# Kernel optimization log

Measured on AMD Instinct MI355X. Metric: run time of the kernel, lower is better.

## Reference

```python
import jax, jax.numpy as jnp
import numpy as np
import math

B, S, HID, NH = 2, 1024, 4096, 32
HD = HID // NH  # 128


def setup_inputs() -> dict:
    key = jax.random.key(0)
    ks = jax.random.split(key, 6)
    scale = 0.02
    x = jax.random.normal(ks[0], (B, S, HID), dtype=jnp.float32)
    Wq = jax.random.normal(ks[1], (HID, HID), dtype=jnp.float32) * scale
    Wk = jax.random.normal(ks[2], (HID, HID), dtype=jnp.float32) * scale
    Wv = jax.random.normal(ks[3], (HID, HID), dtype=jnp.float32) * scale
    Wo = jax.random.normal(ks[4], (HID, HID), dtype=jnp.float32) * scale
    bq = jnp.zeros((HID,), jnp.float32)
    bk = jnp.zeros((HID,), jnp.float32)
    bv = jnp.zeros((HID,), jnp.float32)
    bo = jnp.zeros((HID,), jnp.float32)
    position_ids = jnp.tile(jnp.arange(S, dtype=jnp.int32)[None, :], (B, 1))
    # additive causal mask: 0 on/below diagonal, large negative above
    causal = jnp.tril(jnp.ones((S, S), dtype=bool))
    attention_mask = jnp.where(causal, 0.0, -1e9).astype(jnp.float32)[None, None]
    return {"x": x, "Wq": Wq, "bq": bq, "Wk": Wk, "bk": bk, "Wv": Wv,
            "bv": bv, "Wo": Wo, "bo": bo, "position_ids": position_ids,
            "attention_mask": attention_mask}


def _rotate_interleaved(t):
    # stack([-t[..., 1::2], t[..., ::2]], -1).reshape_as(t)
    return jnp.stack([-t[..., 1::2], t[..., ::2]], axis=-1).reshape(t.shape)


def reference(x, Wq, bq, Wk, bk, Wv, bv, Wo, bo, position_ids, attention_mask):
    b, s, _ = x.shape
    q = x @ Wq.T + bq
    k = x @ Wk.T + bk
    v = x @ Wv.T + bv
    # [B, NH, S, HD]
    q = q.reshape(b, s, NH, HD).transpose(0, 2, 1, 3)
    k = k.reshape(b, s, NH, HD).transpose(0, 2, 1, 3)
    v = v.reshape(b, s, NH, HD).transpose(0, 2, 1, 3)
    # RoPE (interleaved pairs), cos/sin recomputed each call as in source
    inv_freq = 1.0 / (10000.0 ** (jnp.arange(0, HD, 2, dtype=jnp.float32) / HD))
    ang = position_ids.astype(jnp.float32)[..., None] * inv_freq  # [B,S,HD/2]
    cos = jnp.repeat(jnp.cos(ang), 2, axis=-1)[:, None]  # [B,1,S,HD]
    sin = jnp.repeat(jnp.sin(ang), 2, axis=-1)[:, None]
    q = q * cos + _rotate_interleaved(q) * sin
    k = k * cos + _rotate_interleaved(k) * sin
    # naive full attention
    scores = jnp.einsum('bhqd,bhkd->bhqk', q, k) / math.sqrt(HD)
    scores = scores + attention_mask
    probs = jax.nn.softmax(scores, axis=-1)
    out = jnp.einsum('bhqk,bhkd->bhqd', probs, v)
    out = out.transpose(0, 2, 1, 3).reshape(b, s, HID)
    return out @ Wo.T + bo
```

## Files before the change

### kernel.cpp

```cpp
#include <hip/hip_runtime.h>
#include <hip/hip_bf16.h>
#include <cmath>

constexpr int cB  = 2;
constexpr int cS  = 1024;
constexpr int cNH = 32;
constexpr int cHD = 128;
constexpr int cHID = 4096;
constexpr int cM  = cB * cS;

typedef unsigned short u16;
typedef __bf16 bf16x8 __attribute__((ext_vector_type(8)));
typedef float  f32x4  __attribute__((ext_vector_type(4)));

__device__ __forceinline__ u16 f2b(float f) { return __builtin_bit_cast(u16, (__bf16)f); }

__global__ void cvt_bf16(const float* __restrict__ in, u16* __restrict__ out, int n8) {
  int i = blockIdx.x * blockDim.x + threadIdx.x;
  if (i >= n8) return;
  const float4* in4 = (const float4*)in;
  float4 a = in4[2 * i], b = in4[2 * i + 1];
  union { u16 u[8]; uint4 v; } r;
  r.u[0] = f2b(a.x); r.u[1] = f2b(a.y); r.u[2] = f2b(a.z); r.u[3] = f2b(a.w);
  r.u[4] = f2b(b.x); r.u[5] = f2b(b.y); r.u[6] = f2b(b.z); r.u[7] = f2b(b.w);
  ((uint4*)out)[i] = r.v;
}

__global__ void rope_table_k(const int* __restrict__ pos,
                             float* __restrict__ cosT, float* __restrict__ sinT) {
  int idx = blockIdx.x * blockDim.x + threadIdx.x;
  int i = idx & 63, bs = idx >> 6;
  float p = (float)pos[bs];
  float freq = exp2f(-(float)i * (13.287712379549449f / 64.0f));
  float a = p * freq;
  float s, c;
  sincosf(a, &s, &c);
  cosT[idx] = c; sinT[idx] = s;
}

__global__ void rope_apply(u16* __restrict__ Q, u16* __restrict__ Kb,
                           const float* __restrict__ cosT, const float* __restrict__ sinT) {
  int idx = blockIdx.x * blockDim.x + threadIdx.x;
  const int nPer = cB * cS * cNH * (cHD / 8);
  u16* P = (idx < nPer) ? Q : Kb;
  int t = (idx < nPer) ? idx : idx - nPer;
  int d8 = t & 15;
  int h  = (t >> 4) & 31;
  int bs = t >> 9;
  size_t base = ((size_t)bs * cNH + h) * cHD + d8 * 8;
  uint4 v = *reinterpret_cast<uint4*>(P + base);
  u16* u = reinterpret_cast<u16*>(&v);
  int pb = bs * 64 + d8 * 4;
  float4 cs = *reinterpret_cast<const float4*>(cosT + pb);
  float4 sn = *reinterpret_cast<const float4*>(sinT + pb);
  float co[4] = {cs.x, cs.y, cs.z, cs.w};
  float si[4] = {sn.x, sn.y, sn.z, sn.w};
#pragma unroll
  for (int p = 0; p < 4; ++p) {
    float e = (float)__builtin_bit_cast(__bf16, u[2 * p]);
    float o = (float)__builtin_bit_cast(__bf16, u[2 * p + 1]);
    float e2 = e * co[p] - o * si[p];
    float o2 = o * co[p] + e * si[p];
    u[2 * p]     = f2b(e2);
    u[2 * p + 1] = f2b(o2);
  }
  *reinterpret_cast<uint4*>(P + base) = v;
}

__global__ void transpose_v(const u16* __restrict__ V, u16* __restrict__ Vt) {
  __shared__ u16 tile[32][33];
  int bh = blockIdx.z;
  int b = bh >> 5, h = bh & 31;
  int s0 = blockIdx.x * 32, d0 = blockIdx.y * 32;
  int tx = threadIdx.x & 31, ty0 = threadIdx.x >> 5;
#pragma unroll
  for (int i = 0; i < 4; ++i) {
    int r = ty0 + i * 8;
    tile[r][tx] = V[((size_t)(b * cS + s0 + r) * cNH + h) * cHD + d0 + tx];
  }
  __syncthreads();
#pragma unroll
  for (int i = 0; i < 4; ++i) {
    int r = ty0 + i * 8;
    Vt[((size_t)bh * cHD + d0 + r) * cS + s0 + tx] = tile[tx][r];
  }
}

template <int MODE>
__global__ __launch_bounds__(512, 2)
void gemm8(const u16* __restrict__ A,
           const u16* __restrict__ W0, const u16* __restrict__ W1,
           const u16* __restrict__ W2,
           const float* __restrict__ b0, const float* __restrict__ b1,
           const float* __restrict__ b2,
           void* o0, void* o1, void* o2) {
  __shared__ __align__(16) u16 sA[3][128 * 64];
  __shared__ __align__(16) u16 sB[3][256 * 64];
  const int tid = threadIdx.x;
  const int wid = tid >> 6, lane = tid & 63;
  const int c = lane & 15, g = lane >> 4;
  const int wm = wid >> 2, wn = wid & 3;
  const int m0 = blockIdx.x * 128;
  const int gn0 = blockIdx.y * 256;
  const int sel = gn0 >> 12;
  const int n0 = gn0 & 4095;
  const u16* Bw = (sel == 0) ? W0 : (sel == 1 ? W1 : W2);

  f32x4 acc[4][4] = {};
  const int nkt = cHID / 64;

#define STAGE_A(kt, dst)                                                       \
  {                                                                            \
    _Pragma("unroll") for (int l = 0; l < 2; ++l) {                            \
      int chunk = (l * 8 + wid) * 64 + lane;                                   \
      int row = chunk >> 3, kc = (chunk & 7) ^ (row & 7);                      \
      __builtin_amdgcn_global_load_lds(                                        \
          (const void*)(A + (size_t)(m0 + row) * cHID + (kt) * 64 + kc * 8),   \
          (void*)(&sA[dst][(l * 8 + wid) * 512]), 16, 0, 0);                   \
    }                                                                          \
  }
#define STAGE_B(kt, dst)                                                       \
  {                                                                            \
    _Pragma("unroll") for (int l = 0; l < 4; ++l) {                            \
      int chunk = (l * 8 + wid) * 64 + lane;                                   \
      int row = chunk >> 3, kc = (chunk & 7) ^ (row & 7);                      \
      __builtin_amdgcn_global_load_lds(                                        \
          (const void*)(Bw + (size_t)(n0 + row) * cHID + (kt) * 64 + kc * 8),  \
          (void*)(&sB[dst][(l * 8 + wid) * 512]), 16, 0, 0);                   \
    }                                                                          \
  }

  STAGE_A(0, 0); STAGE_B(0, 0);
  STAGE_A(1, 1); STAGE_B(1, 1);
  asm volatile("s_waitcnt vmcnt(6)" ::: "memory");
  __builtin_amdgcn_sched_barrier(0);
  __builtin_amdgcn_s_barrier();
  asm volatile("" ::: "memory");
  __builtin_amdgcn_sched_barrier(0);

  for (int kt = 0; kt < nkt; ++kt) {
    const int bufR = kt % 3;
    const int bufW = (kt + 2) % 3;
    const bool doStage = (kt + 2) < nkt;

    bf16x8 af[4], bw[4];
#pragma unroll
    for (int mf = 0; mf < 4; ++mf) {
      int ra = wm * 64 + mf * 16 + c;
      af[mf] = *reinterpret_cast<const bf16x8*>(
          &sA[bufR][ra * 64 + ((g ^ (ra & 7)) * 8)]);
    }
#pragma unroll
    for (int nf = 0; nf < 4; ++nf) {
      int rb = wn * 64 + nf * 16 + c;
      bw[nf] = *reinterpret_cast<const bf16x8*>(
          &sB[bufR][rb * 64 + ((g ^ (rb & 7)) * 8)]);
    }
    if (doStage) STAGE_A(kt + 2, bufW);
    __builtin_amdgcn_s_setprio(1);
#pragma unroll
    for (int mf = 0; mf < 4; ++mf)
#pragma unroll
      for (int nf = 0; nf < 4; ++nf)
        acc[mf][nf] = __builtin_amdgcn_mfma_f32_16x16x32_bf16(af[mf], bw[nf], acc[mf][nf], 0, 0, 0);
    __builtin_amdgcn_s_setprio(0);

#pragma unroll
    for (int mf = 0; mf < 4; ++mf) {
      int ra = wm * 64 + mf * 16 + c;
      af[mf] = *reinterpret_cast<const bf16x8*>(
          &sA[bufR][ra * 64 + (((4 + g) ^ (ra & 7)) * 8)]);
    }
#pragma unroll
    for (int nf = 0; nf < 4; ++nf) {
      int rb = wn * 64 + nf * 16 + c;
      bw[nf] = *reinterpret_cast<const bf16x8*>(
          &sB[bufR][rb * 64 + (((4 + g) ^ (rb & 7)) * 8)]);
    }
    if (doStage) STAGE_B(kt + 2, bufW);
    __builtin_amdgcn_s_setprio(1);
#pragma unroll
    for (int mf = 0; mf < 4; ++mf)
#pragma unroll
      for (int nf = 0; nf < 4; ++nf)
        acc[mf][nf] = __builtin_amdgcn_mfma_f32_16x16x32_bf16(af[mf], bw[nf], acc[mf][nf], 0, 0, 0);
    __builtin_amdgcn_s_setprio(0);

    if (doStage) {
      asm volatile("s_waitcnt vmcnt(6)" ::: "memory");
    } else {
      asm volatile("s_waitcnt vmcnt(0)" ::: "memory");
    }
    __builtin_amdgcn_sched_barrier(0);
    __builtin_amdgcn_s_barrier();
    asm volatile("" ::: "memory");
    __builtin_amdgcn_sched_barrier(0);
  }
#undef STAGE_A
#undef STAGE_B

  const float* bp = (sel == 0) ? b0 : (sel == 1 ? b1 : b2);
  void* op = (sel == 0) ? o0 : (sel == 1 ? o1 : o2);
#pragma unroll
  for (int nf = 0; nf < 4; ++nf) {
    int col = n0 + wn * 64 + nf * 16 + c;
    float bv = bp[col];
#pragma unroll
    for (int mf = 0; mf < 4; ++mf) {
      int row = m0 + wm * 64 + mf * 16 + g * 4;
#pragma unroll
      for (int r = 0; r < 4; ++r) {
        float v = acc[mf][nf][r] + bv;
        if (MODE == 0)
          ((u16*)op)[(size_t)(row + r) * cHID + col] = f2b(v);
        else
          ((float*)op)[(size_t)(row + r) * cHID + col] = v;
      }
    }
  }
}

__global__ __launch_bounds__(256, 2)
void attn_kernel(const u16* __restrict__ Q, const u16* __restrict__ Kb,
                 const u16* __restrict__ Vt, u16* __restrict__ O) {
  __shared__ __align__(16) char sK[2][16384];
  __shared__ __align__(16) char sV[2][16384];
  __shared__ __align__(16) char sP[8192];
  const int tid = threadIdx.x, w = tid >> 6, lane = tid & 63;
  const int c = lane & 15, g = lane >> 4;
  const int bh = blockIdx.y;
  const int b = bh >> 5, h = bh & 31;
  const int NT = cS / 64;
  const int qtA = blockIdx.x, qtB = NT - 1 - blockIdx.x;
  const float kSc = 0.12751744f;

  bf16x8 qf[2][4];
#pragma unroll
  for (int s = 0; s < 2; ++s) {
    int q0s = (s ? qtA : qtB) * 64;
    size_t qrow = ((size_t)(b * cS + q0s + w * 16 + c) * cNH + h) * cHD;
#pragma unroll
    for (int df = 0; df < 4; ++df)
      qf[s][df] = *reinterpret_cast<const bf16x8*>(Q + qrow + df * 32 + g * 8);
  }

  f32x4 o[2][8] = {};
  float mx[2][4], ls[2][4];
#pragma unroll
  for (int s = 0; s < 2; ++s)
#pragma unroll
    for (int r = 0; r < 4; ++r) { mx[s][r] = -1e30f; ls[s][r] = 0.f; }

  uint4 kv[4], vv[4];
#define LOADT(t)                                                               \
  {                                                                            \
    _Pragma("unroll") for (int i = 0; i < 4; ++i) {                            \
      int cidx = i * 256 + tid;                                                \
      { int row = cidx >> 4, ch = cidx & 15;                                   \
        kv[i] = *reinterpret_cast<const uint4*>(                               \
            Kb + ((size_t)(b * cS + (t) * 64 + row) * cNH + h) * cHD + ch * 8); } \
      { int row = cidx >> 3, ch = cidx & 7;                                    \
        vv[i] = *reinterpret_cast<const uint4*>(                               \
            Vt + ((size_t)bh * cHD + row) * cS + (t) * 64 + ch * 8); }         \
    }                                                                          \
  }
#define WRITET(buf)                                                            \
  {                                                                            \
    _Pragma("unroll") for (int i = 0; i < 4; ++i) {                            \
      int cidx = i * 256 + tid;                                                \
      { int row = cidx >> 4, ch = cidx & 15;                                   \
        *reinterpret_cast<uint4*>(sK[buf] + row * 256 + ((ch ^ (row & 7)) * 16)) = kv[i]; } \
      { int row = cidx >> 3, ch = cidx & 7;                                    \
        *reinterpret_cast<uint4*>(sV[buf] + row * 128 + ((ch ^ (row & 7)) * 16)) = vv[i]; } \
    }                                                                          \
  }

  LOADT(0);
  WRITET(0);
  int cur = 0;

  for (int t = 0; t <= qtB; ++t) {
    __syncthreads();
    if (t < qtB) LOADT(t + 1);

#pragma unroll
    for (int s = 0; s < 2; ++s) {
      const int qt_s = s ? qtA : qtB;
      if (t > qt_s) continue;
      const int q0_s = qt_s * 64;

      f32x4 sc[4] = {};
#pragma unroll
      for (int df = 0; df < 4; ++df) {
        bf16x8 kb[4];
#pragma unroll
        for (int cf = 0; cf < 4; ++cf) {
          int kr = cf * 16 + c;
          kb[cf] = *reinterpret_cast<const bf16x8*>(sK[cur] + kr * 256 + (((df * 4 + g) ^ (kr & 7)) * 16));
        }
#pragma unroll
        for (int cf = 0; cf < 4; ++cf)
          sc[cf] = __builtin_amdgcn_mfma_f32_16x16x32_bf16(qf[s][df], kb[cf], sc[cf], 0, 0, 0);
      }

      if (t == qt_s) {
#pragma unroll
        for (int cf = 0; cf < 4; ++cf) {
          int kg = t * 64 + cf * 16 + c;
#pragma unroll
          for (int r = 0; r < 4; ++r) {
            int qg = q0_s + w * 16 + g * 4 + r;
            if (kg > qg) sc[cf][r] = -1e30f;
          }
        }
      }

      float alpha[4];
#pragma unroll
      for (int r = 0; r < 4; ++r) {
        float v = fmaxf(fmaxf(sc[0][r], sc[1][r]), fmaxf(sc[2][r], sc[3][r]));
        v = fmaxf(v, __shfl_xor(v, 1));
        v = fmaxf(v, __shfl_xor(v, 2));
        v = fmaxf(v, __shfl_xor(v, 4));
        v = fmaxf(v, __shfl_xor(v, 8));
        float mn = fmaxf(mx[s][r], v);
        alpha[r] = exp2f((mx[s][r] - mn) * kSc);
        mx[s][r] = mn;
      }
      float rs[4] = {0.f, 0.f, 0.f, 0.f};
#pragma unroll
      for (int cf = 0; cf < 4; ++cf)
#pragma unroll
        for (int r = 0; r < 4; ++r) {
          float p = exp2f((sc[cf][r] - mx[s][r]) * kSc);
          sc[cf][r] = p;
          rs[r] += p;
        }
#pragma unroll
      for (int r = 0; r < 4; ++r) {
        float v = rs[r];
        v += __shfl_xor(v, 1); v += __shfl_xor(v, 2);
        v += __shfl_xor(v, 4); v += __shfl_xor(v, 8);
        ls[s][r] = ls[s][r] * alpha[r] + v;
      }
#pragma unroll
      for (int nf = 0; nf < 8; ++nf)
#pragma unroll
        for (int r = 0; r < 4; ++r)
          o[s][nf][r] *= alpha[r];

      char* myP = sP + w * 2048;
#pragma unroll
      for (int cf = 0; cf < 4; ++cf) {
        int kcol = cf * 16 + c;
        int chunk = kcol >> 3, within = kcol & 7;
#pragma unroll
        for (int r = 0; r < 4; ++r) {
          int qr = g * 4 + r;
          *reinterpret_cast<u16*>(myP + qr * 128 + ((chunk ^ (qr & 7)) * 16) + within * 2) =
              f2b(sc[cf][r]);
        }
      }
      bf16x8 pa[2];
#pragma unroll
      for (int kf = 0; kf < 2; ++kf)
        pa[kf] = *reinterpret_cast<const bf16x8*>(myP + c * 128 + (((kf * 4 + g) ^ (c & 7)) * 16));

#pragma unroll
      for (int kf = 0; kf < 2; ++kf) {
#pragma unroll
        for (int nf = 0; nf < 8; ++nf) {
          int dr = nf * 16 + c;
          bf16x8 vb = *reinterpret_cast<const bf16x8*>(sV[cur] + dr * 128 + (((kf * 4 + g) ^ (dr & 7)) * 16));
          o[s][nf] = __builtin_amdgcn_mfma_f32_16x16x32_bf16(pa[kf], vb, o[s][nf], 0, 0, 0);
        }
      }
    }

    if (t < qtB) { WRITET(cur ^ 1); cur ^= 1; }
  }

  __syncthreads();
#pragma unroll
  for (int s = 0; s < 2; ++s) {
#pragma unroll
    for (int nf = 0; nf < 8; ++nf) {
#pragma unroll
      for (int r = 0; r < 4; ++r) {
        float v = o[s][nf][r] / ls[s][r];
        int qr = w * 16 + g * 4 + r;
        *reinterpret_cast<u16*>(sK[s] + qr * 256 + (nf * 16 + c) * 2) = f2b(v);
      }
    }
  }
  __syncthreads();
#pragma unroll
  for (int s = 0; s < 2; ++s) {
    int q0_s = (s ? qtA : qtB) * 64;
#pragma unroll
    for (int i = 0; i < 4; ++i) {
      int cidx = i * 256 + tid;
      int row = cidx >> 4, ch = cidx & 15;
      uint4 v = *reinterpret_cast<const uint4*>(sK[s] + row * 256 + ch * 16);
      *reinterpret_cast<uint4*>(O + ((size_t)(b * cS + q0_s + row) * cNH + h) * cHD + ch * 8) = v;
    }
  }
#undef LOADT
#undef WRITET
}

extern "C" void kernel_launch(void* const* d_in, const int* in_sizes, int n_in,
                              void* d_out, int out_size, void* d_ws, size_t ws_size,
                              hipStream_t stream) {
  const float* x  = (const float*)d_in[0];
  const float* Wq = (const float*)d_in[1];
  const float* bq = (const float*)d_in[2];
  const float* Wk = (const float*)d_in[3];
  const float* bk = (const float*)d_in[4];
  const float* Wv = (const float*)d_in[5];
  const float* bv = (const float*)d_in[6];
  const float* Wo = (const float*)d_in[7];
  const float* bo = (const float*)d_in[8];
  const int*  pos = (const int*)d_in[9];
  float* out = (float*)d_out;

  char* ws = (char*)d_ws;
  const size_t MB = 1u << 20;
  const int W8 = (cHID * cHID) / 8;
  const int X8 = (cM * cHID) / 8;
  const int R8 = cB * cS * cNH * (cHD / 8);

  if (ws_size >= 168 * MB) {
    u16* xb  = (u16*)(ws);
    u16* Qb  = (u16*)(ws + 16 * MB);
    u16* Kb  = (u16*)(ws + 32 * MB);
    u16* Vb  = (u16*)(ws + 48 * MB);
    float* cosT = (float*)(ws + 64 * MB);
    float* sinT = cosT + cB * cS * 64;
    u16* WbQ = (u16*)(ws + 72 * MB);
    u16* WbK = (u16*)(ws + 104 * MB);
    u16* WbV = (u16*)(ws + 136 * MB);
    u16* Vt  = WbQ;
    u16* Ab  = WbK;
    u16* WbO = WbV;

    cvt_bf16<<<X8 / 256, 256, 0, stream>>>(x, xb, X8);
    cvt_bf16<<<W8 / 256, 256, 0, stream>>>(Wq, WbQ, W8);
    cvt_bf16<<<W8 / 256, 256, 0, stream>>>(Wk, WbK, W8);
    cvt_bf16<<<W8 / 256, 256, 0, stream>>>(Wv, WbV, W8);
    rope_table_k<<<(cB * cS * 64) / 256, 256, 0, stream>>>(pos, cosT, sinT);

    gemm8<0><<<dim3(16, 48), 512, 0, stream>>>(
        xb, WbQ, WbK, WbV, bq, bk, bv, Qb, Kb, Vb);

    rope_apply<<<(2 * R8) / 256, 256, 0, stream>>>(Qb, Kb, cosT, sinT);
    transpose_v<<<dim3(cS / 32, cHD / 32, cB * cNH), 256, 0, stream>>>(Vb, Vt);
    attn_kernel<<<dim3(cS / 128, cB * cNH), 256, 0, stream>>>(Qb, Kb, Vt, Ab);

    cvt_bf16<<<W8 / 256, 256, 0, stream>>>(Wo, WbO, W8);
    gemm8<1><<<dim3(16, 16), 512, 0, stream>>>(
        Ab, WbO, WbO, WbO, bo, bo, bo, out, out, out);
  } else {
    u16* xb = (u16*)(ws);
    u16* Wb = (u16*)(ws + 16 * MB);
    u16* Qb = (u16*)(ws + 48 * MB);
    u16* Kb = (u16*)(ws + 64 * MB);
    u16* Vb = (u16*)(ws + 80 * MB);
    u16* Vt = xb;
    u16* Ab = Vb;
    float* cosT = (float*)(ws + 96 * MB);
    float* sinT = cosT + cB * cS * 64;

    cvt_bf16<<<X8 / 256, 256, 0, stream>>>(x, xb, X8);
    cvt_bf16<<<W8 / 256, 256, 0, stream>>>(Wq, Wb, W8);
    gemm8<0><<<dim3(16, 16), 512, 0, stream>>>(
        xb, Wb, Wb, Wb, bq, bq, bq, Qb, Qb, Qb);
    cvt_bf16<<<W8 / 256, 256, 0, stream>>>(Wk, Wb, W8);
    gemm8<0><<<dim3(16, 16), 512, 0, stream>>>(
        xb, Wb, Wb, Wb, bk, bk, bk, Kb, Kb, Kb);
    cvt_bf16<<<W8 / 256, 256, 0, stream>>>(Wv, Wb, W8);
    gemm8<0><<<dim3(16, 16), 512, 0, stream>>>(
        xb, Wb, Wb, Wb, bv, bv, bv, Vb, Vb, Vb);

    rope_table_k<<<(cB * cS * 64) / 256, 256, 0, stream>>>(pos, cosT, sinT);
    rope_apply<<<(2 * R8) / 256, 256, 0, stream>>>(Qb, Kb, cosT, sinT);
    transpose_v<<<dim3(cS / 32, cHD / 32, cB * cNH), 256, 0, stream>>>(Vb, Vt);
    attn_kernel<<<dim3(cS / 128, cB * cNH), 256, 0, stream>>>(Qb, Kb, Vt, Ab);

    cvt_bf16<<<W8 / 256, 256, 0, stream>>>(Wo, Wb, W8);
    gemm8<1><<<dim3(16, 16), 512, 0, stream>>>(
        Ab, Wb, Wb, Wb, bo, bo, bo, out, out, out);
  }
}
```

Baseline: 472.8 us.

## Add 256x256-tile GEMM with XCD-aware block mapping and split-K output projection

Replaces the 128x256-tile GEMM with a new 256x256-tile kernel that loads global data straight into LDS with swizzling, double-buffers LDS with explicit waitcnt/barrier scheduling, and maps blocks so that each XCD owns a contiguous group of N tiles. The QKV projection runs as one 384-block launch. The output projection splits K in two, writes fp32 partials to the workspace, and adds a combine_bias kernel that sums them with the bias. The aim is more operand reuse per tile, better L2 locality per XCD, and better occupancy on the smaller output GEMM. The cost is an extra fp32 partial write and read plus one more kernel launch.

```diff
diff --git a/kernel.cpp b/kernel.cpp
--- a/kernel.cpp
+++ b/kernel.cpp
@@ -84,6 +84,176 @@
     int r = ty0 + i * 8;
     Vt[((size_t)bh * cHD + d0 + r) * cS + s0 + tx] = tile[tx][r];
   }
+}
+
+template <int MODE, int NTX>
+__global__ __launch_bounds__(512, 2)
+void gemm256(const u16* __restrict__ A_,
+             const u16* __restrict__ W0, const u16* __restrict__ W1,
+             const u16* __restrict__ W2,
+             const float* __restrict__ b0_, const float* __restrict__ b1_,
+             const float* __restrict__ b2_,
+             void* o0, void* o1, void* o2, int ktiles) {
+  __shared__ __align__(16) u16 sm[2][4][8192];
+  const int tid = threadIdx.x, wid = tid >> 6, lane = tid & 63;
+  const int c = lane & 15, g = lane >> 4;
+  const int wm = wid >> 2, wn = wid & 3;
+  const int gsw = (g ^ ((c >> 1) & 3)) * 8;
+  const int bid = blockIdx.x;
+  const int xcd = bid & 7, j = bid >> 3;
+  const int mt = j / NTX, ntl = xcd * NTX + j % NTX;
+  const int mrow0 = mt * 256;
+  const int gn0 = ntl * 256;
+  const int sel = gn0 >> 12;
+  const int n0 = gn0 & 4095;
+  const u16* Bw = (sel == 0) ? W0 : (sel == 1 ? W1 : W2);
+  const int kbase = blockIdx.y * ktiles * 64;
+
+  f32x4 acc[8][4] = {};
+
+#define STG(P, R0, T, KKH, DD, U)                                              \
+  {                                                                            \
+    _Pragma("unroll") for (int l = 0; l < 2; ++l) {                            \
+      int ci = (l * 8 + wid) * 64 + lane;                                      \
+      int rw = ci >> 2;                                                        \
+      int kc2 = (ci & 3) ^ ((rw >> 1) & 3);                                    \
+      __builtin_amdgcn_global_load_lds(                                        \
+          (const void*)((P) + (size_t)((R0) + rw) * cHID + kbase + (T) * 64 +  \
+                        (KKH) * 32 + kc2 * 8),                                 \
+          (void*)(&sm[DD][U][(l * 8 + wid) * 512]), 16, 0, 0);                 \
+    }                                                                          \
+  }
+
+#define RD_A(dst, MH, UU, DD)                                                  \
+  _Pragma("unroll") for (int i = 0; i < 4; ++i) {                              \
+    int ra = wm * 128 + (MH) * 64 + i * 16 + c;                                \
+    dst[i] = *reinterpret_cast<const bf16x8*>(&sm[DD][UU][ra * 32 + gsw]);     \
+  }
+#define RD_B(dst, UU, DD)                                                      \
+  _Pragma("unroll") for (int i = 0; i < 4; ++i) {                              \
+    int rb = wn * 64 + i * 16 + c;                                             \
+    dst[i] = *reinterpret_cast<const bf16x8*>(&sm[DD][UU][rb * 32 + gsw]);     \
+  }
+#define MFMA16(aR, bR, MOFF)                                                   \
+  __builtin_amdgcn_s_setprio(1);                                               \
+  _Pragma("unroll") for (int i = 0; i < 4; ++i)                                \
+    _Pragma("unroll") for (int nf = 0; nf < 4; ++nf)                           \
+      acc[(MOFF) + i][nf] =                                                    \
+          __builtin_amdgcn_mfma_f32_16x16x32_bf16(aR[i], bR[nf],               \
+                                                  acc[(MOFF) + i][nf], 0, 0, 0); \
+  __builtin_amdgcn_s_setprio(0);
+#define LEADBAR                                                                \
+  __builtin_amdgcn_s_barrier();                                                \
+  asm volatile("s_waitcnt lgkmcnt(0)" ::: "memory");                           \
+  __builtin_amdgcn_sched_barrier(0)
+#define TRAILBAR                                                               \
+  __builtin_amdgcn_s_barrier();                                                \
+  __builtin_amdgcn_sched_barrier(0)
+
+#define GTILE(DD, KT, SON, LAST)                                               \
+  {                                                                            \
+    bf16x8 aR[4], bk0[4], bk1[4];                                              \
+                                                   \
+    RD_A(aR, 0, 0, DD); RD_B(bk0, 1, DD);                                      \
+    if (SON) STG(A_, mrow0, (KT) + 1, 0, (DD) ^ 1, 0);                         \
+    LEADBAR;                                                                   \
+    MFMA16(aR, bk0, 0);                                                        \
+    TRAILBAR;                                                                  \
+                                                   \
+    RD_A(aR, 1, 0, DD);                                                        \
+    if (SON) STG(Bw, n0, (KT) + 1, 0, (DD) ^ 1, 1);                            \
+    LEADBAR;                                                                   \
+    MFMA16(aR, bk0, 4);                                                        \
+    if (LAST) { asm volatile("s_waitcnt vmcnt(0)" ::: "memory"); }             \
+    else      { asm volatile("s_waitcnt vmcnt(4)" ::: "memory"); }             \
+    __builtin_amdgcn_sched_barrier(0);                                         \
+    TRAILBAR;                                                                  \
+                                                   \
+    RD_A(aR, 0, 2, DD); RD_B(bk1, 3, DD);                                      \
+    if (SON) STG(A_, mrow0, (KT) + 1, 1, (DD) ^ 1, 2);                         \
+    LEADBAR;                                                                   \
+    MFMA16(aR, bk1, 0);                                                        \
+    TRAILBAR;                                                                  \
+                                                   \
+    RD_A(aR, 1, 2, DD);                                                        \
+    if (SON) STG(Bw, n0, (KT) + 1, 1, (DD) ^ 1, 3);                            \
+    LEADBAR;                                                                   \
+    MFMA16(aR, bk1, 4);                                                        \
+    if (SON) {                                                                 \
+      asm volatile("s_waitcnt vmcnt(4)" ::: "memory");                         \
+      __builtin_amdgcn_sched_barrier(0);                                       \
+    }                                                                          \
+    TRAILBAR;                                                                  \
+  }
+
+  STG(A_, mrow0, 0, 0, 0, 0);
+  STG(Bw, n0, 0, 0, 0, 1);
+  STG(A_, mrow0, 0, 1, 0, 2);
+  STG(Bw, n0, 0, 1, 0, 3);
+  asm volatile("s_waitcnt vmcnt(4)" ::: "memory");
+  __builtin_amdgcn_sched_barrier(0);
+  __builtin_amdgcn_s_barrier();
+  __builtin_amdgcn_sched_barrier(0);
+
+  for (int kt = 0; kt < ktiles - 1; ++kt) {
+    const int D = kt & 1;
+    GTILE(D, kt, 1, 0);
+  }
+  {
+    const int D = (ktiles - 1) & 1;
+    GTILE(D, ktiles - 1, 0, 1);
+  }
+#undef GTILE
+#undef STG
+#undef RD_A
+#undef RD_B
+#undef MFMA16
+#undef LEADBAR
+#undef TRAILBAR
+
+  const float* bp = (sel == 0) ? b0_ : (sel == 1 ? b1_ : b2_);
+  void* op = (sel == 0) ? o0 : (sel == 1 ? o1 : o2);
+  if (MODE == 0) {
+#pragma unroll
+    for (int nf = 0; nf < 4; ++nf) {
+      int col = n0 + wn * 64 + nf * 16 + c;
+      float bv = bp[col];
+#pragma unroll
+      for (int mf = 0; mf < 8; ++mf) {
+        int row = mrow0 + wm * 128 + mf * 16 + g * 4;
+#pragma unroll
+        for (int r = 0; r < 4; ++r)
+          ((u16*)op)[(size_t)(row + r) * cHID + col] = f2b(acc[mf][nf][r] + bv);
+      }
+    }
+  } else {
+    float* fp = (float*)op + (size_t)blockIdx.y * cM * cHID;
+#pragma unroll
+    for (int nf = 0; nf < 4; ++nf) {
+      int col = n0 + wn * 64 + nf * 16 + c;
+#pragma unroll
+      for (int mf = 0; mf < 8; ++mf) {
+        int row = mrow0 + wm * 128 + mf * 16 + g * 4;
+#pragma unroll
+        for (int r = 0; r < 4; ++r)
+          fp[(size_t)(row + r) * cHID + col] = acc[mf][nf][r];
+      }
+    }
+  }
+}
+
+__global__ void combine_bias(const float* __restrict__ P,
+                             const float* __restrict__ bias,
+                             float* __restrict__ out) {
+  int i = blockIdx.x * blockDim.x + threadIdx.x;
+  float4 a = ((const float4*)P)[i];
+  float4 b = ((const float4*)P)[i + (cM * cHID / 4)];
+  int col4 = (i & (cHID / 4 - 1)) * 4;
+  float4 bb = *reinterpret_cast<const float4*>(bias + col4);
+  float4 r;
+  r.x = a.x + b.x + bb.x; r.y = a.y + b.y + bb.y;
+  r.z = a.z + b.z + bb.z; r.w = a.w + b.w + bb.w;
+  ((float4*)out)[i] = r;
 }
 
 template <int MODE>
@@ -443,6 +613,7 @@
     u16* Vt  = WbQ;
     u16* Ab  = WbK;
     u16* WbO = WbV;
+    float* P01 = (float*)(ws);
 
     cvt_bf16<<<X8 / 256, 256, 0, stream>>>(x, xb, X8);
     cvt_bf16<<<W8 / 256, 256, 0, stream>>>(Wq, WbQ, W8);
@@ -450,16 +621,17 @@
     cvt_bf16<<<W8 / 256, 256, 0, stream>>>(Wv, WbV, W8);
     rope_table_k<<<(cB * cS * 64) / 256, 256, 0, stream>>>(pos, cosT, sinT);
 
-    gemm8<0><<<dim3(16, 48), 512, 0, stream>>>(
-        xb, WbQ, WbK, WbV, bq, bk, bv, Qb, Kb, Vb);
+    gemm256<0, 6><<<dim3(384), 512, 0, stream>>>(
+        xb, WbQ, WbK, WbV, bq, bk, bv, Qb, Kb, Vb, 64);
 
     rope_apply<<<(2 * R8) / 256, 256, 0, stream>>>(Qb, Kb, cosT, sinT);
     transpose_v<<<dim3(cS / 32, cHD / 32, cB * cNH), 256, 0, stream>>>(Vb, Vt);
     attn_kernel<<<dim3(cS / 128, cB * cNH), 256, 0, stream>>>(Qb, Kb, Vt, Ab);
 
     cvt_bf16<<<W8 / 256, 256, 0, stream>>>(Wo, WbO, W8);
-    gemm8<1><<<dim3(16, 16), 512, 0, stream>>>(
-        Ab, WbO, WbO, WbO, bo, bo, bo, out, out, out);
+    gemm256<2, 2><<<dim3(128, 2), 512, 0, stream>>>(
+        Ab, WbO, WbO, WbO, nullptr, nullptr, nullptr, P01, P01, P01, 32);
+    combine_bias<<<(cM * cHID / 4) / 256, 256, 0, stream>>>(P01, bo, out);
   } else {
     u16* xb = (u16*)(ws);
     u16* Wb = (u16*)(ws + 16 * MB);
```

New measurement: 503.6 us. 6.5% more time.
